# Kernel optimization log

Hardware: AMD Instinct MI355X
Metric: run time of the kernel (lower is better)

Reference implementation:

```python
import jax, jax.numpy as jnp
import numpy as np
import math

D_MODEL = 1024
NUM_HEADS = 16
HEAD_DIM = D_MODEL // NUM_HEADS
THETA = 10000.0
B, S = 2, 2048


def _rope(x, positions, theta):
    # x: (b, h, s, d); positions: (s,) int
    d = x.shape[-1]
    inv_freq = theta ** (-jnp.arange(0, d, 2, dtype=jnp.float32) / d)  # (d/2,)
    ang = positions.astype(jnp.float32)[:, None] * inv_freq[None, :]   # (s, d/2)
    cos, sin = jnp.cos(ang), jnp.sin(ang)
    x1 = x[..., ::2]
    x2 = x[..., 1::2]
    r1 = x1 * cos - x2 * sin
    r2 = x1 * sin + x2 * cos
    # interleave back to (..., d)
    return jnp.stack([r1, r2], axis=-1).reshape(x.shape)


def setup_inputs() -> dict:
    key = jax.random.key(0)
    ks = jax.random.split(key, 5)
    std = math.sqrt(2.0 / (D_MODEL + D_MODEL))
    return {
        "x": jax.random.normal(ks[0], (B, S, D_MODEL), dtype=jnp.float32),
        "token_positions": jnp.arange(S, dtype=jnp.int32),
        "Wq": jax.random.normal(ks[1], (D_MODEL, D_MODEL), dtype=jnp.float32) * std,
        "Wk": jax.random.normal(ks[2], (D_MODEL, D_MODEL), dtype=jnp.float32) * std,
        "Wv": jax.random.normal(ks[3], (D_MODEL, D_MODEL), dtype=jnp.float32) * std,
        "Wo": jax.random.normal(ks[4], (D_MODEL, D_MODEL), dtype=jnp.float32) * std,
    }


def reference(x, token_positions, Wq, Wk, Wv, Wo):
    b, s, _ = x.shape
    def split_heads(t):
        return t.reshape(b, s, NUM_HEADS, HEAD_DIM).transpose(0, 2, 1, 3)  # (b,h,s,d)
    Q = split_heads(x @ Wq.T)
    K = split_heads(x @ Wk.T)
    V = split_heads(x @ Wv.T)
    Q = _rope(Q, token_positions, THETA)
    K = _rope(K, token_positions, THETA)
    scores = jnp.einsum("bhqd,bhkd->bhqk", Q, K) / math.sqrt(HEAD_DIM)
    causal = jnp.tril(jnp.ones((s, s), dtype=bool))
    scores = jnp.where(causal, scores, -jnp.inf)
    attn = jax.nn.softmax(scores, axis=-1)
    out = jnp.einsum("bhqk,bhkd->bhqd", attn, V)
    out = out.transpose(0, 2, 1, 3).reshape(b, s, D_MODEL)
    return out @ Wo.T
```

## Files before the change

kernel.cpp:

```cpp
#include <hip/hip_runtime.h>
#include <math.h>

typedef unsigned short u16;
typedef unsigned int   u32;
typedef __attribute__((ext_vector_type(8))) short bf16x8;
typedef __attribute__((ext_vector_type(4))) float floatx4;
typedef __attribute__((ext_vector_type(4))) _Float16 halfx4;
typedef __attribute__((ext_vector_type(2))) unsigned int uintx2;

#define SEQ 2048
#define DM  1024
#define NH  16
#define DH  64
#define MM  4096
#define QSCALE 0.18033688011112042f

__device__ __forceinline__ u16 f2bf(float f) {
    u32 u = __builtin_bit_cast(u32, f);
    u += 0x7fffu + ((u >> 16) & 1u);
    return (u16)(u >> 16);
}

__device__ __forceinline__ void async16(const void* g, void* l) {
    __builtin_amdgcn_global_load_lds(
        (const __attribute__((address_space(1))) void*)g,
        (__attribute__((address_space(3))) void*)l, 16, 0, 0);
}

__global__ __launch_bounds__(256) void prep_kernel(const float* __restrict__ x,
                                                   const float* __restrict__ w0,
                                                   const float* __restrict__ w1,
                                                   const float* __restrict__ w2,
                                                   const float* __restrict__ w3,
                                                   u16* __restrict__ Xsh,
                                                   u16* __restrict__ Wsh,
                                                   const int* __restrict__ pos,
                                                   float2* __restrict__ tab) {
    const int bid = blockIdx.x, cb = blockIdx.y, tid = threadIdx.x;

    int lin = bid * 16 + cb;
    if (lin < 256) {
        int i = lin * 256 + tid;
        int p = i >> 5, d2 = i & 31;
        float freq = __expf(-(float)d2 * (9.2103403719761836f / 32.0f));
        float sv, cv;
        sincosf((float)pos[p] * freq, &sv, &cv);
        tab[i] = make_float2(cv, sv);
    }

    const float* src; u16* dst; int row0;
    if (bid < 64) { src = x; dst = Xsh; row0 = bid * 64; }
    else {
        int wi = (bid - 64) >> 4;
        src = (wi == 0) ? w0 : (wi == 1) ? w1 : (wi == 2) ? w2 : w3;
        dst = Wsh + (size_t)wi * DM * DM;
        row0 = ((bid - 64) & 15) * 64;
    }
    __shared__ __align__(16) u16 t[64 * 64];
#pragma unroll
    for (int rep = 0; rep < 4; ++rep) {
        int f = rep * 256 + tid;
        int r = f >> 4, c4 = f & 15;
        float4 v = *(const float4*)&src[(size_t)(row0 + r) * DM + cb * 64 + c4 * 4];
        uint2 pk;
        pk.x = (u32)f2bf(v.x) | ((u32)f2bf(v.y) << 16);
        pk.y = (u32)f2bf(v.z) | ((u32)f2bf(v.w) << 16);
        int ch = (c4 >> 1) ^ (r & 7);
        *(uint2*)&t[r * 64 + ch * 8 + (c4 & 1) * 4] = pk;
    }
    __syncthreads();
#pragma unroll
    for (int rep = 0; rep < 2; ++rep) {
        int s = rep * 256 + tid;
        int tile = s >> 6, l = s & 63;
        int mt = tile >> 1, kt = tile & 1, lm = l & 15, quad = l >> 4;
        int m = mt * 16 + lm;
        uint4 v = *(const uint4*)&t[m * 64 + ((kt * 4 + quad) ^ (m & 7)) * 8];
        size_t rowblk = (size_t)(row0 >> 4) + mt;
        size_t ktile  = cb * 2 + kt;
        *(uint4*)&dst[(rowblk * 32 + ktile) * 512 + l * 8] = v;
    }
}

template<int NZ, bool OUTF32>
__global__ __launch_bounds__(256, 2) void gemm_f(const u16* __restrict__ Ash,
                                                 const u16* __restrict__ Wbase,
                                                 u16* __restrict__ outbf,
                                                 float* __restrict__ outf,
                                                 _Float16* __restrict__ vtout,
                                                 const float2* __restrict__ ropetab) {
    const int m0 = blockIdx.x * 64, n0 = blockIdx.y * 128;
    const int tid = threadIdx.x, lane = tid & 63, w = tid >> 6;
    const int lm = lane & 15, quad = lane >> 4;
    const int rb0 = m0 >> 4;
    const int cb0 = n0 >> 4;

    __shared__ __align__(16) u16 lsA[2][4 * 512];
    __shared__ __align__(16) u16 lsB[2][NZ * 8 * 512];

    const u16* aSrc = Ash + ((size_t)(rb0 + w) * 32) * 512 + lane * 8;
    constexpr int NPW = NZ * 2;
    const u16* bSrc[NPW];
#pragma unroll
    for (int j = 0; j < NPW; ++j) {
        int p = w * NPW + j, z = p >> 3, cb8 = p & 7;
        bSrc[j] = Wbase + (size_t)z * (DM * DM)
                + ((size_t)(cb0 + cb8) * 32) * 512 + lane * 8;
    }

    auto stage = [&](int buf, int it) {
        async16(aSrc + (size_t)it * 512, &lsA[buf][w * 512 + lane * 8]);
#pragma unroll
        for (int j = 0; j < NPW; ++j)
            async16(bSrc[j] + (size_t)it * 512,
                    &lsB[buf][(w * NPW + j) * 512 + lane * 8]);
    };

    floatx4 acc[NZ][4][2];
    const floatx4 z4 = {0.f, 0.f, 0.f, 0.f};
#pragma unroll
    for (int z = 0; z < NZ; ++z)
#pragma unroll
        for (int mt = 0; mt < 4; ++mt)
#pragma unroll
            for (int nt = 0; nt < 2; ++nt) acc[z][mt][nt] = z4;

    stage(0, 0);
    __syncthreads();

#pragma unroll 2
    for (int it = 0; it < 32; ++it) {
        if (it < 31) stage((it + 1) & 1, it + 1);
        const u16* La = &lsA[it & 1][0];
        const u16* Lb = &lsB[it & 1][0];
        bf16x8 a[4], b[NZ][2];
#pragma unroll
        for (int mt = 0; mt < 4; ++mt)
            a[mt] = *(const bf16x8*)&La[mt * 512 + lane * 8];
#pragma unroll
        for (int z = 0; z < NZ; ++z)
#pragma unroll
            for (int nt = 0; nt < 2; ++nt)
                b[z][nt] = *(const bf16x8*)&Lb[(z * 8 + w * 2 + nt) * 512 + lane * 8];
#pragma unroll
        for (int z = 0; z < NZ; ++z)
#pragma unroll
            for (int mt = 0; mt < 4; ++mt)
#pragma unroll
                for (int nt = 0; nt < 2; ++nt)
                    acc[z][mt][nt] = __builtin_amdgcn_mfma_f32_16x16x32_bf16(
                        a[mt], b[z][nt], acc[z][mt][nt], 0, 0, 0);
        __syncthreads();
    }

#pragma unroll
    for (int z = 0; z < NZ; ++z) {
        if (!OUTF32 && NZ == 3 && z == 2) {
#pragma unroll
            for (int mt = 0; mt < 4; ++mt) {
                int row = m0 + mt * 16 + quad * 4;
                int b = row >> 11, s = row & (SEQ - 1);
#pragma unroll
                for (int nt = 0; nt < 2; ++nt) {
                    int col = n0 + w * 32 + nt * 16 + lm;
                    uint2 pk;
                    pk.x = __builtin_bit_cast(u32, __builtin_amdgcn_cvt_pkrtz(acc[z][mt][nt][0], acc[z][mt][nt][1]));
                    pk.y = __builtin_bit_cast(u32, __builtin_amdgcn_cvt_pkrtz(acc[z][mt][nt][2], acc[z][mt][nt][3]));
                    *(uint2*)&vtout[((size_t)b * NH * DH + (size_t)col) * SEQ + s] = pk;
                }
            }
            continue;
        }
        const bool rope = !OUTF32;
        const float osc = (!OUTF32 && z == 0) ? QSCALE : 1.0f;
#pragma unroll
        for (int mt = 0; mt < 4; ++mt)
#pragma unroll
            for (int r = 0; r < 4; ++r) {
                int row = m0 + mt * 16 + quad * 4 + r;
#pragma unroll
                for (int nt = 0; nt < 2; ++nt) {
                    int col = n0 + w * 32 + nt * 16 + lm;
                    float v  = acc[z][mt][nt][r];
                    if (rope) {
                        float pv = __shfl_xor(v, 1);
                        float2 cs = ropetab[(row & (SEQ - 1)) * 32 + ((col & 63) >> 1)];
                        v = (lm & 1) ? fmaf(pv, cs.y, v * cs.x) : fmaf(v, cs.x, -pv * cs.y);
                    }
                    v *= osc;
                    if (OUTF32) {
                        outf[(size_t)row * DM + col] = v;
                    } else {
                        float hv = __shfl_xor(v, 1);
                        if (!(lm & 1)) {
                            u32 pk = (u32)f2bf(v) | ((u32)f2bf(hv) << 16);
                            *(u32*)&outbf[(size_t)z * ((size_t)MM * DM) + (size_t)row * DM + col] = pk;
                        }
                    }
                }
            }
    }
}

__global__ __launch_bounds__(512) void attn_kernel(const u16* __restrict__ Q,
                                                   const u16* __restrict__ K,
                                                   const _Float16* __restrict__ Vt,
                                                   u16* __restrict__ AO) {
    const int u  = blockIdx.x;
    const int qt = (u < 256) ? (15 - (u >> 5)) : ((u >> 5) - 8);
    const int bh = u & 31;
    const int b  = bh >> 4, h = bh & 15;
    const int q0 = qt * 128;
    const int tid = threadIdx.x, w = tid >> 6, lane = tid & 63;
    const int lm = lane & 15, quad = lane >> 4;

    __shared__ __align__(16) u16      lsK[2][128 * 64];
    __shared__ __align__(16) _Float16 lsV[2][64 * 128];

    bf16x8 qb[2];
#pragma unroll
    for (int ks = 0; ks < 2; ++ks)
        qb[ks] = *(const bf16x8*)
            &Q[(size_t)(b * SEQ + q0 + w * 16 + lm) * DM + h * DH + ks * 32 + quad * 8];

    const floatx4 z4 = {0.f, 0.f, 0.f, 0.f};
    floatx4 o[4];
#pragma unroll
    for (int dt = 0; dt < 4; ++dt) o[dt] = z4;
    float lsum = 0.f;

    const int qloc = w * 16 + lm;

    auto stageKV = [&](int buf, int kt) {
#pragma unroll
        for (int rep = 0; rep < 2; ++rep) {
            int f = rep * 512 + tid;
            int krow = f >> 3, kcb = (f & 7) ^ (krow & 7);
            async16(&K[(size_t)(b * SEQ + kt * 128 + krow) * DM + h * DH + kcb * 8],
                    &lsK[buf][f * 8]);
            int d = f >> 4, gbs = (f & 15) ^ ((d >> 1) & 7);
            async16(&Vt[(size_t)(bh * DH + d) * SEQ + kt * 128 + gbs * 8],
                    &lsV[buf][f * 8]);
        }
    };

    stageKV(0, 0);
    for (int kt = 0; kt <= qt; ++kt) {
        __syncthreads();
        if (kt < qt) stageKV((kt + 1) & 1, kt + 1);
        const u16*      Lk = lsK[kt & 1];
        const _Float16* Lv = lsV[kt & 1];

        floatx4 s4[8];
#pragma unroll
        for (int st = 0; st < 8; ++st) s4[st] = z4;
#pragma unroll
        for (int ks = 0; ks < 2; ++ks) {
            const int cbl = ((ks * 4 + quad) ^ (lm & 7)) * 8;
#pragma unroll
            for (int st = 0; st < 8; ++st) {
                bf16x8 ka = *(const bf16x8*)&Lk[(st * 16 + lm) * 64 + cbl];
                s4[st] = __builtin_amdgcn_mfma_f32_16x16x32_bf16(ka, qb[ks], s4[st], 0, 0, 0);
            }
        }

        halfx4 pb[8];
        const bool diag = (kt == qt);
#pragma unroll
        for (int st = 0; st < 8; ++st) {
#pragma unroll
            for (int r = 0; r < 4; ++r) {
                float v = s4[st][r];
                if (diag) {
                    int keyloc = st * 16 + quad * 4 + r;
                    if (keyloc > qloc) v = -1e30f;
                }
                v = exp2f(v);
                lsum += v;
                s4[st][r] = v;
            }
            uintx2 pk2;
            pk2.x = __builtin_bit_cast(u32, __builtin_amdgcn_cvt_pkrtz(s4[st][0], s4[st][1]));
            pk2.y = __builtin_bit_cast(u32, __builtin_amdgcn_cvt_pkrtz(s4[st][2], s4[st][3]));
            pb[st] = __builtin_bit_cast(halfx4, pk2);
        }

#pragma unroll
        for (int st = 0; st < 8; ++st) {
#pragma unroll
            for (int dt = 0; dt < 4; ++dt) {
                int drow = dt * 16 + lm;
                int sbs = (st * 2 + (quad >> 1)) ^ ((drow >> 1) & 7);
                halfx4 va = *(const halfx4*)&Lv[drow * 128 + sbs * 8 + (quad & 1) * 4];
                o[dt] = __builtin_amdgcn_mfma_f32_16x16x16f16(va, pb[st], o[dt], 0, 0, 0);
            }
        }
    }

    lsum += __shfl_xor(lsum, 16);
    lsum += __shfl_xor(lsum, 32);
    float rl = 1.0f / lsum;

    __syncthreads();
    u16* eb = (u16*)&lsK[0][0];
    const int q = w * 16 + lm;
#pragma unroll
    for (int dt = 0; dt < 4; ++dt) {
        uint2 pk;
        pk.x = (u32)f2bf(o[dt][0] * rl) | ((u32)f2bf(o[dt][1] * rl) << 16);
        pk.y = (u32)f2bf(o[dt][2] * rl) | ((u32)f2bf(o[dt][3] * rl) << 16);
        int ch = (dt * 2 + (quad >> 1)) ^ (lm & 7);
        *(uint2*)&eb[q * 64 + ch * 8 + (quad & 1) * 4] = pk;
    }
    __syncthreads();
    const size_t rowblk = (size_t)((b * SEQ + q0) >> 4) + w;
#pragma unroll
    for (int kt = 0; kt < 2; ++kt) {
        uint4 v = *(const uint4*)&eb[(w * 16 + lm) * 64 + ((kt * 4 + quad) ^ (lm & 7)) * 8];
        *(uint4*)&AO[(rowblk * 32 + (h * 2 + kt)) * 512 + lane * 8] = v;
    }
}

extern "C" void kernel_launch(void* const* d_in, const int* in_sizes, int n_in,
                              void* d_out, int out_size, void* d_ws, size_t ws_size,
                              hipStream_t stream) {
    const float* x   = (const float*)d_in[0];
    const int*   pos = (const int*)d_in[1];
    float* out = (float*)d_out;

    u16* ws = (u16*)d_ws;
    const size_t MD = (size_t)MM * DM;
    const size_t DD = (size_t)DM * DM;
    u16* Xsh = ws;
    u16* Wsh = ws + MD;
    u16* Qbf = ws + MD + 4 * DD;
    u16* Kbf = Qbf + MD;
    u16* VtB = Kbf + MD;
    float2* ropetab = (float2*)(VtB + MD);
    _Float16* Vt = (_Float16*)VtB;
    u16* AOsh = Xsh;

    prep_kernel<<<dim3(128, 16), 256, 0, stream>>>(
        x, (const float*)d_in[2], (const float*)d_in[3], (const float*)d_in[4],
        (const float*)d_in[5], Xsh, Wsh, pos, ropetab);

    gemm_f<3, false><<<dim3(64, 8), 256, 0, stream>>>(
        Xsh, Wsh, Qbf, nullptr, Vt, ropetab);

    attn_kernel<<<dim3(512), 512, 0, stream>>>(Qbf, Kbf, Vt, AOsh);

    gemm_f<1, true><<<dim3(64, 8), 256, 0, stream>>>(
        AOsh, Wsh + 3 * DD, nullptr, out, nullptr, ropetab);
}
```

Measured before the change: 192.2 us.

## Process two query sub-tiles per wave in attention to reuse K/V fragments

```diff
diff --git a/kernel.cpp b/kernel.cpp
--- a/kernel.cpp
+++ b/kernel.cpp
@@ -202,10 +202,10 @@
     }
 }
 
-__global__ __launch_bounds__(512) void attn_kernel(const u16* __restrict__ Q,
-                                                   const u16* __restrict__ K,
-                                                   const _Float16* __restrict__ Vt,
-                                                   u16* __restrict__ AO) {
+__global__ __launch_bounds__(256, 2) void attn_kernel(const u16* __restrict__ Q,
+                                                      const u16* __restrict__ K,
+                                                      const _Float16* __restrict__ Vt,
+                                                      u16* __restrict__ AO) {
     const int u  = blockIdx.x;
     const int qt = (u < 256) ? (15 - (u >> 5)) : ((u >> 5) - 8);
     const int bh = u & 31;
@@ -217,24 +217,26 @@
     __shared__ __align__(16) u16      lsK[2][128 * 64];
     __shared__ __align__(16) _Float16 lsV[2][64 * 128];
 
-    bf16x8 qb[2];
-#pragma unroll
-    for (int ks = 0; ks < 2; ++ks)
-        qb[ks] = *(const bf16x8*)
-            &Q[(size_t)(b * SEQ + q0 + w * 16 + lm) * DM + h * DH + ks * 32 + quad * 8];
+    bf16x8 qb[2][2];
+#pragma unroll
+    for (int qi = 0; qi < 2; ++qi)
+#pragma unroll
+        for (int ks = 0; ks < 2; ++ks)
+            qb[qi][ks] = *(const bf16x8*)
+                &Q[(size_t)(b * SEQ + q0 + w * 32 + qi * 16 + lm) * DM + h * DH + ks * 32 + quad * 8];
 
     const floatx4 z4 = {0.f, 0.f, 0.f, 0.f};
-    floatx4 o[4];
-#pragma unroll
-    for (int dt = 0; dt < 4; ++dt) o[dt] = z4;
-    float lsum = 0.f;
-
-    const int qloc = w * 16 + lm;
+    floatx4 o[2][4];
+#pragma unroll
+    for (int qi = 0; qi < 2; ++qi)
+#pragma unroll
+        for (int dt = 0; dt < 4; ++dt) o[qi][dt] = z4;
+    float lsum[2] = {0.f, 0.f};
 
     auto stageKV = [&](int buf, int kt) {
 #pragma unroll
-        for (int rep = 0; rep < 2; ++rep) {
-            int f = rep * 512 + tid;
+        for (int rep = 0; rep < 4; ++rep) {
+            int f = rep * 256 + tid;
             int krow = f >> 3, kcb = (f & 7) ^ (krow & 7);
             async16(&K[(size_t)(b * SEQ + kt * 128 + krow) * DM + h * DH + kcb * 8],
                     &lsK[buf][f * 8]);
@@ -251,73 +253,88 @@
         const u16*      Lk = lsK[kt & 1];
         const _Float16* Lv = lsV[kt & 1];
 
-        floatx4 s4[8];
-#pragma unroll
-        for (int st = 0; st < 8; ++st) s4[st] = z4;
+        floatx4 s4[2][8];
+#pragma unroll
+        for (int qi = 0; qi < 2; ++qi)
+#pragma unroll
+            for (int st = 0; st < 8; ++st) s4[qi][st] = z4;
 #pragma unroll
         for (int ks = 0; ks < 2; ++ks) {
             const int cbl = ((ks * 4 + quad) ^ (lm & 7)) * 8;
 #pragma unroll
             for (int st = 0; st < 8; ++st) {
                 bf16x8 ka = *(const bf16x8*)&Lk[(st * 16 + lm) * 64 + cbl];
-                s4[st] = __builtin_amdgcn_mfma_f32_16x16x32_bf16(ka, qb[ks], s4[st], 0, 0, 0);
-            }
-        }
-
-        halfx4 pb[8];
+#pragma unroll
+                for (int qi = 0; qi < 2; ++qi)
+                    s4[qi][st] = __builtin_amdgcn_mfma_f32_16x16x32_bf16(ka, qb[qi][ks], s4[qi][st], 0, 0, 0);
+            }
+        }
+
         const bool diag = (kt == qt);
 #pragma unroll
         for (int st = 0; st < 8; ++st) {
-#pragma unroll
-            for (int r = 0; r < 4; ++r) {
-                float v = s4[st][r];
-                if (diag) {
-                    int keyloc = st * 16 + quad * 4 + r;
-                    if (keyloc > qloc) v = -1e30f;
+            halfx4 pb2[2];
+#pragma unroll
+            for (int qi = 0; qi < 2; ++qi) {
+#pragma unroll
+                for (int r = 0; r < 4; ++r) {
+                    float v = s4[qi][st][r];
+                    if (diag) {
+                        int keyloc = st * 16 + quad * 4 + r;
+                        if (keyloc > w * 32 + qi * 16 + lm) v = -1e30f;
+                    }
+                    v = exp2f(v);
+                    lsum[qi] += v;
+                    s4[qi][st][r] = v;
                 }
-                v = exp2f(v);
-                lsum += v;
-                s4[st][r] = v;
-            }
-            uintx2 pk2;
-            pk2.x = __builtin_bit_cast(u32, __builtin_amdgcn_cvt_pkrtz(s4[st][0], s4[st][1]));
-            pk2.y = __builtin_bit_cast(u32, __builtin_amdgcn_cvt_pkrtz(s4[st][2], s4[st][3]));
-            pb[st] = __builtin_bit_cast(halfx4, pk2);
-        }
-
-#pragma unroll
-        for (int st = 0; st < 8; ++st) {
+                uintx2 pk2;
+                pk2.x = __builtin_bit_cast(u32, __builtin_amdgcn_cvt_pkrtz(s4[qi][st][0], s4[qi][st][1]));
+                pk2.y = __builtin_bit_cast(u32, __builtin_amdgcn_cvt_pkrtz(s4[qi][st][2], s4[qi][st][3]));
+                pb2[qi] = __builtin_bit_cast(halfx4, pk2);
+            }
 #pragma unroll
             for (int dt = 0; dt < 4; ++dt) {
                 int drow = dt * 16 + lm;
                 int sbs = (st * 2 + (quad >> 1)) ^ ((drow >> 1) & 7);
                 halfx4 va = *(const halfx4*)&Lv[drow * 128 + sbs * 8 + (quad & 1) * 4];
-                o[dt] = __builtin_amdgcn_mfma_f32_16x16x16f16(va, pb[st], o[dt], 0, 0, 0);
-            }
-        }
-    }
-
-    lsum += __shfl_xor(lsum, 16);
-    lsum += __shfl_xor(lsum, 32);
-    float rl = 1.0f / lsum;
+#pragma unroll
+                for (int qi = 0; qi < 2; ++qi)
+                    o[qi][dt] = __builtin_amdgcn_mfma_f32_16x16x16f16(va, pb2[qi], o[qi][dt], 0, 0, 0);
+            }
+        }
+    }
+
+    float rl[2];
+#pragma unroll
+    for (int qi = 0; qi < 2; ++qi) {
+        lsum[qi] += __shfl_xor(lsum[qi], 16);
+        lsum[qi] += __shfl_xor(lsum[qi], 32);
+        rl[qi] = 1.0f / lsum[qi];
+    }
 
     __syncthreads();
     u16* eb = (u16*)&lsK[0][0];
-    const int q = w * 16 + lm;
-#pragma unroll
-    for (int dt = 0; dt < 4; ++dt) {
-        uint2 pk;
-        pk.x = (u32)f2bf(o[dt][0] * rl) | ((u32)f2bf(o[dt][1] * rl) << 16);
-        pk.y = (u32)f2bf(o[dt][2] * rl) | ((u32)f2bf(o[dt][3] * rl) << 16);
-        int ch = (dt * 2 + (quad >> 1)) ^ (lm & 7);
-        *(uint2*)&eb[q * 64 + ch * 8 + (quad & 1) * 4] = pk;
+#pragma unroll
+    for (int qi = 0; qi < 2; ++qi) {
+        const int q = w * 32 + qi * 16 + lm;
+#pragma unroll
+        for (int dt = 0; dt < 4; ++dt) {
+            uint2 pk;
+            pk.x = (u32)f2bf(o[qi][dt][0] * rl[qi]) | ((u32)f2bf(o[qi][dt][1] * rl[qi]) << 16);
+            pk.y = (u32)f2bf(o[qi][dt][2] * rl[qi]) | ((u32)f2bf(o[qi][dt][3] * rl[qi]) << 16);
+            int ch = (dt * 2 + (quad >> 1)) ^ (lm & 7);
+            *(uint2*)&eb[q * 64 + ch * 8 + (quad & 1) * 4] = pk;
+        }
     }
     __syncthreads();
-    const size_t rowblk = (size_t)((b * SEQ + q0) >> 4) + w;
-#pragma unroll
-    for (int kt = 0; kt < 2; ++kt) {
-        uint4 v = *(const uint4*)&eb[(w * 16 + lm) * 64 + ((kt * 4 + quad) ^ (lm & 7)) * 8];
-        *(uint4*)&AO[(rowblk * 32 + (h * 2 + kt)) * 512 + lane * 8] = v;
+    const size_t rowblk0 = (size_t)((b * SEQ + q0) >> 4);
+#pragma unroll
+    for (int rbi = 0; rbi < 2; ++rbi) {
+#pragma unroll
+        for (int kt = 0; kt < 2; ++kt) {
+            uint4 v = *(const uint4*)&eb[((w * 2 + rbi) * 16 + lm) * 64 + ((kt * 4 + quad) ^ (lm & 7)) * 8];
+            *(uint4*)&AO[((rowblk0 + w * 2 + rbi) * 32 + (h * 2 + kt)) * 512 + lane * 8] = v;
+        }
     }
 }
 
@@ -347,7 +364,7 @@
     gemm_f<3, false><<<dim3(64, 8), 256, 0, stream>>>(
         Xsh, Wsh, Qbf, nullptr, Vt, ropetab);
 
-    attn_kernel<<<dim3(512), 512, 0, stream>>>(Qbf, Kbf, Vt, AOsh);
+    attn_kernel<<<dim3(512), 256, 0, stream>>>(Qbf, Kbf, Vt, AOsh);
 
     gemm_f<1, true><<<dim3(64, 8), 256, 0, stream>>>(
         AOsh, Wsh + 3 * DD, nullptr, out, nullptr, ropetab);
```

Measured after the change: 187.3 us. 1.03x faster.
